# Kernel tuning notes

Measured on AMD Instinct MI355X. Metric: run time of the kernel, lower is better.

## Reference

```python
import jax, jax.numpy as jnp
import numpy as np

BATCH, T, N_INP, N_HID = 32, 512, 128, 1024
DT = 0.042
RHO = 0.99
INPUT_SCALING = 1.0
THRESHOLD = 0.5
RESET = 0.0
R_ = 1.0   # resistance
C_ = 1.0   # capacity
P = 0.5
HARMONIC = N_HID * P          # scalar, as in source: n_hid * p
SPIKING = N_HID - HARMONIC    # scalar, as in source


def setup_inputs() -> dict:
    key = jax.random.key(0)
    k1, k2, k3, k4, k5 = jax.random.split(key, 5)
    x = jax.random.normal(k1, (BATCH, T, N_INP), dtype=jnp.float32)
    # input-to-hidden in (0, input_scaling), per torch.rand * input_scaling
    x2h = jax.random.uniform(k2, (N_INP, N_HID), dtype=jnp.float32) * INPUT_SCALING
    # hidden-to-hidden: full topology, rescaled to spectral radius rho
    W = np.asarray(jax.random.uniform(k3, (N_HID, N_HID), minval=-1.0, maxval=1.0))
    sr = float(np.max(np.abs(np.linalg.eigvals(W))))
    h2h = jnp.asarray(W * (RHO / sr), dtype=jnp.float32)
    # gamma/epsilon sampled per-unit from uniform ranges (tuple branch of __init__)
    gamma = jax.random.uniform(k4, (N_HID,), minval=0.5, maxval=1.5, dtype=jnp.float32)
    epsilon = jax.random.uniform(k5, (N_HID,), minval=0.001, maxval=0.01, dtype=jnp.float32)
    bias = jnp.zeros((N_HID,), dtype=jnp.float32)
    return {"x": x, "x2h": x2h, "h2h": h2h, "gamma": gamma, "epsilon": epsilon, "bias": bias}


def reference(x, x2h, h2h, gamma, epsilon, bias):
    B = x.shape[0]
    dtype = x.dtype
    u_decay = 1.0 - R_ * C_ * DT  # u = u + R*C*dt*(-u)

    def step(carry, xt):
        hy, hz, u = carry
        # spiking_osc: threshold, reset, leak
        spike = (u > THRESHOLD).astype(dtype)
        u = jnp.where(spike == 1.0, RESET, u)
        u = u * u_decay
        # coupled-oscillator update
        drive = jnp.tanh(xt @ x2h + hy @ h2h + bias)
        hz = hz + DT * (drive - gamma * hy - (epsilon * (hz * HARMONIC) + u * SPIKING))
        hy = hy + DT * hz
        return (hy, hz, u), (hy, hz, u, spike)

    zeros = jnp.zeros((B, N_HID), dtype=dtype)
    (_, _, _), (hy_t, hz_t, u_t, spk_t) = jax.lax.scan(
        step, (zeros, zeros, zeros), jnp.swapaxes(x, 0, 1)
    )
    # (T, B, H) -> (B, T, H), matching the per-step lists of the original
    tr = lambda a: jnp.swapaxes(a, 0, 1)
    return tr(hy_t), tr(hz_t), tr(u_t), tr(spk_t)
```

## Files before the change

### kernel.cpp

```cpp
#include <hip/hip_runtime.h>
#include <cmath>

constexpr int  Bn  = 32, Tn = 512, NIn = 128, Hn = 1024;
constexpr long long TH  = (long long)Tn * Hn;
constexpr long long BTH = (long long)Bn * TH;
constexpr float DTc  = 0.042f;
constexpr float UDEC = 1.0f - 1.0f * 1.0f * DTc;
constexpr float HARM = 512.0f;
constexpr float SPIK = 512.0f;

__device__ unsigned g_tag[16 * 32 * 16];

__global__ void init_tag() {
    int i = threadIdx.x;
    __hip_atomic_store(&g_tag[i * 16], 0u,
                       __ATOMIC_RELAXED, __HIP_MEMORY_SCOPE_AGENT);
}

__global__ __launch_bounds__(256) void pre_gemm(const float* __restrict__ x,
                                                const float* __restrict__ x2h,
                                                const float* __restrict__ bias,
                                                float* __restrict__ pre) {
    __shared__ float xs[64 * 128];
    __shared__ float ws[128 * 64];
    const int tid = threadIdx.x;
    const int rb  = blockIdx.y * 64;
    const int cb  = blockIdx.x * 64;

#pragma unroll
    for (int i = 0; i < 8; ++i) {
        int idx = i * 1024 + tid * 4;
        int r = idx >> 7, k = idx & 127;
        *(float4*)(&xs[r * 128 + k]) =
            *(const float4*)(&x[(long long)(rb + r) * NIn + k]);
    }
#pragma unroll
    for (int i = 0; i < 8; ++i) {
        int idx = i * 1024 + tid * 4;
        int k = idx >> 6, c = idx & 63;
        *(float4*)(&ws[k * 64 + c]) =
            *(const float4*)(&x2h[(long long)k * Hn + cb + c]);
    }
    __syncthreads();

    const int tx = tid & 15, ty = tid >> 4;
    const int r0 = ty * 4, c0 = tx * 4;
    float acc[4][4] = {};
#pragma unroll 4
    for (int k = 0; k < 128; ++k) {
        float4 bv = *(const float4*)(&ws[k * 64 + c0]);
        float a0 = xs[(r0 + 0) * 128 + k];
        float a1 = xs[(r0 + 1) * 128 + k];
        float a2 = xs[(r0 + 2) * 128 + k];
        float a3 = xs[(r0 + 3) * 128 + k];
        acc[0][0] += a0 * bv.x; acc[0][1] += a0 * bv.y; acc[0][2] += a0 * bv.z; acc[0][3] += a0 * bv.w;
        acc[1][0] += a1 * bv.x; acc[1][1] += a1 * bv.y; acc[1][2] += a1 * bv.z; acc[1][3] += a1 * bv.w;
        acc[2][0] += a2 * bv.x; acc[2][1] += a2 * bv.y; acc[2][2] += a2 * bv.z; acc[2][3] += a2 * bv.w;
        acc[3][0] += a3 * bv.x; acc[3][1] += a3 * bv.y; acc[3][2] += a3 * bv.z; acc[3][3] += a3 * bv.w;
    }
    float4 bb = *(const float4*)(&bias[cb + c0]);
#pragma unroll
    for (int i = 0; i < 4; ++i) {
        float4 o;
        o.x = acc[i][0] + bb.x; o.y = acc[i][1] + bb.y;
        o.z = acc[i][2] + bb.z; o.w = acc[i][3] + bb.w;
        *(float4*)(&pre[(long long)(rb + r0 + i) * Hn + cb + c0]) = o;
    }
}

__global__ __launch_bounds__(512, 1) void ron_loop8(const float* __restrict__ h2h,
                                                    const float* __restrict__ gam,
                                                    const float* __restrict__ eps,
                                                    float* __restrict__ out) {
    extern __shared__ float sm[];
    float* hyl  = sm;
    float* wt   = sm + 4 * 1028;
    float* part = wt;

    const int tid = threadIdx.x;
    const int bx  = blockIdx.x;
    const int bg  = bx & 7;
    const int hg  = bx >> 3;
    const int c0  = hg * 32;
    const int b0  = bg * 4;
    unsigned* mytag   = &g_tag[(bg * 32 + hg) * 16];
    unsigned* tagbase = &g_tag[bg * 32 * 16];

    float* hy_o = out;
    float* hz_o = out + BTH;
    float* u_o  = out + 2 * BTH;
    float* sp_o = out + 3 * BTH;

    for (int idx = tid; idx < 32 * 1024; idx += 512) {
        int cc2 = idx & 31, k = idx >> 5;
        wt[cc2 * 1028 + k] = h2h[(long long)k * Hn + c0 + cc2];
    }
    __syncthreads();

    const int ks   = tid & 63;
    const int tile = tid >> 6;

    float4 W[4][4];
#pragma unroll
    for (int j = 0; j < 4; ++j)
#pragma unroll
        for (int m = 0; m < 4; ++m)
            W[j][m] = *(const float4*)(wt + (tile * 4 + j) * 1028 + m * 256 + ks * 4);

    const float* hp0 = hyl + ks * 4;
    const float* hp1 = hp0 + 1028;
    const float* hp2 = hp0 + 2 * 1028;
    const float* hp3 = hp0 + 3 * 1028;
    float* pw = part + (tile * 4) * 65 + ks;

    const int r  = tid & 127;
    const int cc = r & 31;
    const int bb = r >> 5;
    const int b  = b0 + bb;
    const int h  = c0 + cc;
    const float g = gam[h];
    const float e = eps[h];
    float hy = 0.0f, hz = 0.0f, u = 0.0f;

#define D4(dst, hv, wv)                                         \
    dst = fmaf(hv.x, wv.x, dst); dst = fmaf(hv.y, wv.y, dst);   \
    dst = fmaf(hv.z, wv.z, dst); dst = fmaf(hv.w, wv.w, dst)

    for (int t = 0; t < Tn; ++t) {
        float pre_v = 0.0f;
        if (tid < 128)
            pre_v = u_o[(long long)b * TH + (long long)t * Hn + h];

        float acc = 0.0f;
        if (t > 0) {
            const long long base = (long long)b0 * TH + (long long)(t - 1) * Hn + tid;
            float v[8];
#pragma unroll
            for (int i = 0; i < 8; ++i) {
                v[i] = __hip_atomic_load(
                    &hy_o[base + (long long)(i >> 1) * TH + (i & 1) * 512],
                    __ATOMIC_RELAXED, __HIP_MEMORY_SCOPE_AGENT);
            }
#pragma unroll
            for (int i = 0; i < 8; ++i)
                hyl[(i >> 1) * 1028 + (i & 1) * 512 + tid] = v[i];
            __syncthreads();

            float a00 = 0.f, a01 = 0.f, a02 = 0.f, a03 = 0.f;
            float a10 = 0.f, a11 = 0.f, a12 = 0.f, a13 = 0.f;
            float a20 = 0.f, a21 = 0.f, a22 = 0.f, a23 = 0.f;
            float a30 = 0.f, a31 = 0.f, a32 = 0.f, a33 = 0.f;
#pragma unroll
            for (int m = 0; m < 4; ++m) {
                const int o4 = m * 256;
                float4 h0 = *(const float4*)(hp0 + o4);
                float4 h1 = *(const float4*)(hp1 + o4);
                float4 h2 = *(const float4*)(hp2 + o4);
                float4 h3 = *(const float4*)(hp3 + o4);
                D4(a00, h0, W[0][m]); D4(a01, h0, W[1][m]); D4(a02, h0, W[2][m]); D4(a03, h0, W[3][m]);
                D4(a10, h1, W[0][m]); D4(a11, h1, W[1][m]); D4(a12, h1, W[2][m]); D4(a13, h1, W[3][m]);
                D4(a20, h2, W[0][m]); D4(a21, h2, W[1][m]); D4(a22, h2, W[2][m]); D4(a23, h2, W[3][m]);
                D4(a30, h3, W[0][m]); D4(a31, h3, W[1][m]); D4(a32, h3, W[2][m]); D4(a33, h3, W[3][m]);
            }

            pw[(0 * 32 + 0) * 65] = a00; pw[(0 * 32 + 1) * 65] = a01;
            pw[(0 * 32 + 2) * 65] = a02; pw[(0 * 32 + 3) * 65] = a03;
            pw[(1 * 32 + 0) * 65] = a10; pw[(1 * 32 + 1) * 65] = a11;
            pw[(1 * 32 + 2) * 65] = a12; pw[(1 * 32 + 3) * 65] = a13;
            pw[(2 * 32 + 0) * 65] = a20; pw[(2 * 32 + 1) * 65] = a21;
            pw[(2 * 32 + 2) * 65] = a22; pw[(2 * 32 + 3) * 65] = a23;
            pw[(3 * 32 + 0) * 65] = a30; pw[(3 * 32 + 1) * 65] = a31;
            pw[(3 * 32 + 2) * 65] = a32; pw[(3 * 32 + 3) * 65] = a33;
            __syncthreads();

            if (tid < 128) {
                const float* pr = part + r * 65;
                float s0 = 0.f, s1 = 0.f, s2 = 0.f, s3 = 0.f;
#pragma unroll
                for (int k = 0; k < 64; k += 4) {
                    s0 += pr[k + 0]; s1 += pr[k + 1];
                    s2 += pr[k + 2]; s3 += pr[k + 3];
                }
                acc = (s0 + s1) + (s2 + s3);
            }
        }

        float spike = 0.0f;
        long long o = 0;
        if (tid < 128) {
            spike = (u > 0.5f) ? 1.0f : 0.0f;
            u = (spike == 1.0f) ? 0.0f : u;
            u = u * UDEC;
            float drive = tanhf(acc + pre_v);
            hz = hz + DTc * (drive - g * hy - (e * (hz * HARM) + u * SPIK));
            hy = hy + DTc * hz;
            o = (long long)b * TH + (long long)t * Hn + h;
            __hip_atomic_store(&hy_o[o], hy,
                               __ATOMIC_RELAXED, __HIP_MEMORY_SCOPE_AGENT);
        }

        if (t < Tn - 1) {
            __syncthreads();
            if (tid == 0)
                __hip_atomic_store(mytag, (unsigned)(t + 1),
                                   __ATOMIC_RELAXED, __HIP_MEMORY_SCOPE_AGENT);
        }

        if (tid < 128) {
            hz_o[o] = hz;
            u_o[o]  = u;
            sp_o[o] = spike;
        }

        if (t < Tn - 1) {
            if (tid < 64) {
                const unsigned target = (unsigned)(t + 1);
                const int idx = tid & 31;
                for (;;) {
                    unsigned v = __hip_atomic_load(&tagbase[idx * 16],
                                                   __ATOMIC_RELAXED,
                                                   __HIP_MEMORY_SCOPE_AGENT);
                    if (__ballot(v < target) == 0ull) break;
                }
            }
            __syncthreads();
        }
    }
#undef D4
}

__global__ __launch_bounds__(256, 1) void ron_loop4(const float* __restrict__ h2h,
                                                    const float* __restrict__ gam,
                                                    const float* __restrict__ eps,
                                                    float* __restrict__ out) {
    extern __shared__ float sm[];
    float* hyl  = sm;
    float* wt   = sm + 4 * 1028;
    float* part = wt;

    const int tid = threadIdx.x;
    const int bx  = blockIdx.x;
    const int bg  = bx & 7;
    const int hg  = bx >> 3;
    const int c0  = hg * 32;
    const int b0  = bg * 4;
    unsigned* mytag   = &g_tag[(bg * 32 + hg) * 16];
    unsigned* tagbase = &g_tag[bg * 32 * 16];

    float* hy_o = out;
    float* hz_o = out + BTH;
    float* u_o  = out + 2 * BTH;
    float* sp_o = out + 3 * BTH;

    for (int idx = tid; idx < 32 * 1024; idx += 256) {
        int cc2 = idx & 31, k = idx >> 5;
        wt[cc2 * 1028 + k] = h2h[(long long)k * Hn + c0 + cc2];
    }
    __syncthreads();

    const int ks   = tid & 31;
    const int tile = tid >> 5;

    float4 W[4][8];
#pragma unroll
    for (int j = 0; j < 4; ++j)
#pragma unroll
        for (int m = 0; m < 8; ++m)
            W[j][m] = *(const float4*)(wt + (tile * 4 + j) * 1028 + (ks + 32 * m) * 4);

    const float* hp0 = hyl + ks * 4;
    const float* hp1 = hp0 + 1028;
    const float* hp2 = hp0 + 2 * 1028;
    const float* hp3 = hp0 + 3 * 1028;
    float* pw = part + (tile * 4) * 33 + ks;

    const int r  = tid & 127;
    const int cc = r & 31;
    const int bb = r >> 5;
    const int b  = b0 + bb;
    const int h  = c0 + cc;
    const float g = gam[h];
    const float e = eps[h];
    float hy = 0.0f, hz = 0.0f, u = 0.0f;

#define D4(dst, hv, wv)                                         \
    dst = fmaf(hv.x, wv.x, dst); dst = fmaf(hv.y, wv.y, dst);   \
    dst = fmaf(hv.z, wv.z, dst); dst = fmaf(hv.w, wv.w, dst)

    for (int t = 0; t < Tn; ++t) {
        float pre_v = 0.0f;
        if (tid < 128)
            pre_v = u_o[(long long)b * TH + (long long)t * Hn + h];

        float acc = 0.0f;
        if (t > 0) {
            const long long base = (long long)b0 * TH + (long long)(t - 1) * Hn + tid;
            float v[16];
#pragma unroll
            for (int i = 0; i < 16; ++i) {
                v[i] = __hip_atomic_load(
                    &hy_o[base + (long long)(i >> 2) * TH + (i & 3) * 256],
                    __ATOMIC_RELAXED, __HIP_MEMORY_SCOPE_AGENT);
            }
#pragma unroll
            for (int i = 0; i < 16; ++i)
                hyl[(i >> 2) * 1028 + (i & 3) * 256 + tid] = v[i];
            __syncthreads();

            float a00 = 0.f, a01 = 0.f, a02 = 0.f, a03 = 0.f;
            float a10 = 0.f, a11 = 0.f, a12 = 0.f, a13 = 0.f;
            float a20 = 0.f, a21 = 0.f, a22 = 0.f, a23 = 0.f;
            float a30 = 0.f, a31 = 0.f, a32 = 0.f, a33 = 0.f;
#pragma unroll
            for (int m = 0; m < 8; ++m) {
                const int o4 = m * 128;
                float4 h0 = *(const float4*)(hp0 + o4);
                float4 h1 = *(const float4*)(hp1 + o4);
                float4 h2 = *(const float4*)(hp2 + o4);
                float4 h3 = *(const float4*)(hp3 + o4);
                D4(a00, h0, W[0][m]); D4(a01, h0, W[1][m]); D4(a02, h0, W[2][m]); D4(a03, h0, W[3][m]);
                D4(a10, h1, W[0][m]); D4(a11, h1, W[1][m]); D4(a12, h1, W[2][m]); D4(a13, h1, W[3][m]);
                D4(a20, h2, W[0][m]); D4(a21, h2, W[1][m]); D4(a22, h2, W[2][m]); D4(a23, h2, W[3][m]);
                D4(a30, h3, W[0][m]); D4(a31, h3, W[1][m]); D4(a32, h3, W[2][m]); D4(a33, h3, W[3][m]);
            }

            pw[(0 * 32 + 0) * 33] = a00; pw[(0 * 32 + 1) * 33] = a01;
            pw[(0 * 32 + 2) * 33] = a02; pw[(0 * 32 + 3) * 33] = a03;
            pw[(1 * 32 + 0) * 33] = a10; pw[(1 * 32 + 1) * 33] = a11;
            pw[(1 * 32 + 2) * 33] = a12; pw[(1 * 32 + 3) * 33] = a13;
            pw[(2 * 32 + 0) * 33] = a20; pw[(2 * 32 + 1) * 33] = a21;
            pw[(2 * 32 + 2) * 33] = a22; pw[(2 * 32 + 3) * 33] = a23;
            pw[(3 * 32 + 0) * 33] = a30; pw[(3 * 32 + 1) * 33] = a31;
            pw[(3 * 32 + 2) * 33] = a32; pw[(3 * 32 + 3) * 33] = a33;
            __syncthreads();

            if (tid < 128) {
                const float* pr = part + r * 33;
                float s0 = 0.f, s1 = 0.f, s2 = 0.f, s3 = 0.f;
#pragma unroll
                for (int k = 0; k < 32; k += 4) {
                    s0 += pr[k + 0]; s1 += pr[k + 1];
                    s2 += pr[k + 2]; s3 += pr[k + 3];
                }
                acc = (s0 + s1) + (s2 + s3);
            }
        }

        float spike = 0.0f;
        long long o = 0;
        if (tid < 128) {
            spike = (u > 0.5f) ? 1.0f : 0.0f;
            u = (spike == 1.0f) ? 0.0f : u;
            u = u * UDEC;
            float drive = tanhf(acc + pre_v);
            hz = hz + DTc * (drive - g * hy - (e * (hz * HARM) + u * SPIK));
            hy = hy + DTc * hz;
            o = (long long)b * TH + (long long)t * Hn + h;
            __hip_atomic_store(&hy_o[o], hy,
                               __ATOMIC_RELAXED, __HIP_MEMORY_SCOPE_AGENT);
        }

        if (t < Tn - 1) {
            __syncthreads();
            if (tid == 0)
                __hip_atomic_store(mytag, (unsigned)(t + 1),
                                   __ATOMIC_RELAXED, __HIP_MEMORY_SCOPE_AGENT);
        }

        if (tid < 128) {
            hz_o[o] = hz;
            u_o[o]  = u;
            sp_o[o] = spike;
        }

        if (t < Tn - 1) {
            if (tid < 64) {
                const unsigned target = (unsigned)(t + 1);
                const int idx = tid & 31;
                for (;;) {
                    unsigned v = __hip_atomic_load(&tagbase[idx * 16],
                                                   __ATOMIC_RELAXED,
                                                   __HIP_MEMORY_SCOPE_AGENT);
                    if (__ballot(v < target) == 0ull) break;
                    __builtin_amdgcn_s_sleep(1);
                }
            }
            __syncthreads();
        }
    }
#undef D4
}

extern "C" void kernel_launch(void* const* d_in, const int* in_sizes, int n_in,
                              void* d_out, int out_size, void* d_ws, size_t ws_size,
                              hipStream_t stream) {
    const float* x    = (const float*)d_in[0];
    const float* x2h  = (const float*)d_in[1];
    const float* h2h  = (const float*)d_in[2];
    const float* gam  = (const float*)d_in[3];
    const float* eps  = (const float*)d_in[4];
    const float* bias = (const float*)d_in[5];
    float* out = (float*)d_out;
    float* pre = out + 2 * BTH;

    init_tag<<<1, 512, 0, stream>>>();
    pre_gemm<<<dim3(16, 256), dim3(256), 0, stream>>>(x, x2h, bias, pre);

    const unsigned smem = (4 * 1028 + 32 * 1028) * sizeof(float);
    (void)hipFuncSetAttribute((const void*)ron_loop8,
                              hipFuncAttributeMaxDynamicSharedMemorySize,
                              (int)smem);
    (void)hipFuncSetAttribute((const void*)ron_loop4,
                              hipFuncAttributeMaxDynamicSharedMemorySize,
                              (int)smem);

    void* args[] = {(void*)&h2h, (void*)&gam, (void*)&eps, (void*)&out};

    bool launched =
        (hipLaunchCooperativeKernel((void*)ron_loop8, dim3(256), dim3(512),
                                    args, smem, stream) == hipSuccess);
    if (!launched) {
        (void)hipLaunchCooperativeKernel((void*)ron_loop4, dim3(256),
                                         dim3(256), args, smem, stream);
    }
}
```

Measured before the change: 1.961 ms.

## Replace tag barrier with per-element tagged hy exchange buffer

```diff
diff --git a/kernel.cpp b/kernel.cpp
--- a/kernel.cpp
+++ b/kernel.cpp
@@ -9,12 +9,16 @@
 constexpr float HARM = 512.0f;
 constexpr float SPIK = 512.0f;
 
+__device__ unsigned long long g_ex[2][8][4][1024];
+
 __device__ unsigned g_tag[16 * 32 * 16];
 
-__global__ void init_tag() {
-    int i = threadIdx.x;
-    __hip_atomic_store(&g_tag[i * 16], 0u,
-                       __ATOMIC_RELAXED, __HIP_MEMORY_SCOPE_AGENT);
+__global__ void init_ex() {
+    int i = blockIdx.x * 256 + threadIdx.x;
+    ((unsigned long long*)g_ex)[i] = 0xFFFFFFFF00000000ULL;
+    if (i < 16 * 32)
+        __hip_atomic_store(&g_tag[i * 16], 0u,
+                           __ATOMIC_RELAXED, __HIP_MEMORY_SCOPE_AGENT);
 }
 
 __global__ __launch_bounds__(256) void pre_gemm(const float* __restrict__ x,
@@ -68,6 +72,167 @@
     }
 }
 
+__global__ __launch_bounds__(512, 1) void ron_fuse(const float* __restrict__ h2h,
+                                                   const float* __restrict__ gam,
+                                                   const float* __restrict__ eps,
+                                                   float* __restrict__ out) {
+    extern __shared__ float sm[];
+    float* hyl  = sm;
+    float* wt   = sm + 4 * 1028;
+    float* part = wt;
+
+    const int tid = threadIdx.x;
+    const int bx  = blockIdx.x;
+    const int bg  = bx & 7;
+    const int hg  = bx >> 3;
+    const int c0  = hg * 32;
+    const int b0  = bg * 4;
+
+    float* hy_o = out;
+    float* hz_o = out + BTH;
+    float* u_o  = out + 2 * BTH;
+    float* sp_o = out + 3 * BTH;
+
+    for (int idx = tid; idx < 32 * 1024; idx += 512) {
+        int cc2 = idx & 31, k = idx >> 5;
+        wt[cc2 * 1028 + k] = h2h[(long long)k * Hn + c0 + cc2];
+    }
+    __syncthreads();
+
+    const int ks   = tid & 63;
+    const int tile = tid >> 6;
+
+    float4 W[4][4];
+#pragma unroll
+    for (int j = 0; j < 4; ++j)
+#pragma unroll
+        for (int m = 0; m < 4; ++m)
+            W[j][m] = *(const float4*)(wt + (tile * 4 + j) * 1028 + m * 256 + ks * 4);
+
+    const float* hp0 = hyl + ks * 4;
+    const float* hp1 = hp0 + 1028;
+    const float* hp2 = hp0 + 2 * 1028;
+    const float* hp3 = hp0 + 3 * 1028;
+    float* pw = part + (tile * 4) * 65 + ks;
+
+    const int r  = tid & 127;
+    const int cc = r & 31;
+    const int bb = r >> 5;
+    const int b  = b0 + bb;
+    const int h  = c0 + cc;
+    const float g = gam[h];
+    const float e = eps[h];
+    float hy = 0.0f, hz = 0.0f, u = 0.0f;
+
+#define D4(dst, hv, wv)                                         \
+    dst = fmaf(hv.x, wv.x, dst); dst = fmaf(hv.y, wv.y, dst);   \
+    dst = fmaf(hv.z, wv.z, dst); dst = fmaf(hv.w, wv.w, dst)
+
+    for (int t = 0; t < Tn; ++t) {
+        float pre_v = 0.0f;
+        if (tid < 128)
+            pre_v = u_o[(long long)b * TH + (long long)t * Hn + h];
+
+        float acc = 0.0f;
+        if (t > 0) {
+            const int par = (t - 1) & 1;
+            const unsigned want = (unsigned)(t - 1);
+            unsigned long long w[8];
+            float fv[8];
+            unsigned got = 0;
+#pragma unroll
+            for (int i = 0; i < 8; ++i)
+                w[i] = __hip_atomic_load(
+                    &g_ex[par][bg][i >> 1][(i & 1) * 512 + tid],
+                    __ATOMIC_RELAXED, __HIP_MEMORY_SCOPE_AGENT);
+#pragma unroll
+            for (int i = 0; i < 8; ++i)
+                if ((unsigned)(w[i] >> 32) == want) {
+                    fv[i] = __uint_as_float((unsigned)w[i]);
+                    got |= 1u << i;
+                }
+            while (got != 0xFFu) {
+#pragma unroll
+                for (int i = 0; i < 8; ++i) {
+                    if (!(got & (1u << i))) {
+                        unsigned long long v = __hip_atomic_load(
+                            &g_ex[par][bg][i >> 1][(i & 1) * 512 + tid],
+                            __ATOMIC_RELAXED, __HIP_MEMORY_SCOPE_AGENT);
+                        if ((unsigned)(v >> 32) == want) {
+                            fv[i] = __uint_as_float((unsigned)v);
+                            got |= 1u << i;
+                        }
+                    }
+                }
+            }
+#pragma unroll
+            for (int i = 0; i < 8; ++i)
+                hyl[(i >> 1) * 1028 + (i & 1) * 512 + tid] = fv[i];
+            __syncthreads();
+
+            float a00 = 0.f, a01 = 0.f, a02 = 0.f, a03 = 0.f;
+            float a10 = 0.f, a11 = 0.f, a12 = 0.f, a13 = 0.f;
+            float a20 = 0.f, a21 = 0.f, a22 = 0.f, a23 = 0.f;
+            float a30 = 0.f, a31 = 0.f, a32 = 0.f, a33 = 0.f;
+#pragma unroll
+            for (int m = 0; m < 4; ++m) {
+                const int o4 = m * 256;
+                float4 h0 = *(const float4*)(hp0 + o4);
+                float4 h1 = *(const float4*)(hp1 + o4);
+                float4 h2 = *(const float4*)(hp2 + o4);
+                float4 h3 = *(const float4*)(hp3 + o4);
+                D4(a00, h0, W[0][m]); D4(a01, h0, W[1][m]); D4(a02, h0, W[2][m]); D4(a03, h0, W[3][m]);
+                D4(a10, h1, W[0][m]); D4(a11, h1, W[1][m]); D4(a12, h1, W[2][m]); D4(a13, h1, W[3][m]);
+                D4(a20, h2, W[0][m]); D4(a21, h2, W[1][m]); D4(a22, h2, W[2][m]); D4(a23, h2, W[3][m]);
+                D4(a30, h3, W[0][m]); D4(a31, h3, W[1][m]); D4(a32, h3, W[2][m]); D4(a33, h3, W[3][m]);
+            }
+
+            pw[(0 * 32 + 0) * 65] = a00; pw[(0 * 32 + 1) * 65] = a01;
+            pw[(0 * 32 + 2) * 65] = a02; pw[(0 * 32 + 3) * 65] = a03;
+            pw[(1 * 32 + 0) * 65] = a10; pw[(1 * 32 + 1) * 65] = a11;
+            pw[(1 * 32 + 2) * 65] = a12; pw[(1 * 32 + 3) * 65] = a13;
+            pw[(2 * 32 + 0) * 65] = a20; pw[(2 * 32 + 1) * 65] = a21;
+            pw[(2 * 32 + 2) * 65] = a22; pw[(2 * 32 + 3) * 65] = a23;
+            pw[(3 * 32 + 0) * 65] = a30; pw[(3 * 32 + 1) * 65] = a31;
+            pw[(3 * 32 + 2) * 65] = a32; pw[(3 * 32 + 3) * 65] = a33;
+            __syncthreads();
+
+            if (tid < 128) {
+                const float* pr = part + r * 65;
+                float s0 = 0.f, s1 = 0.f, s2 = 0.f, s3 = 0.f;
+#pragma unroll
+                for (int k = 0; k < 64; k += 4) {
+                    s0 += pr[k + 0]; s1 += pr[k + 1];
+                    s2 += pr[k + 2]; s3 += pr[k + 3];
+                }
+                acc = (s0 + s1) + (s2 + s3);
+            }
+        }
+
+        if (tid < 128) {
+            float spike = (u > 0.5f) ? 1.0f : 0.0f;
+            u = (spike == 1.0f) ? 0.0f : u;
+            u = u * UDEC;
+            float drive = tanhf(acc + pre_v);
+            hz = hz + DTc * (drive - g * hy - (e * (hz * HARM) + u * SPIK));
+            hy = hy + DTc * hz;
+            if (t < Tn - 1) {
+                unsigned long long pk =
+                    ((unsigned long long)(unsigned)t << 32) |
+                    (unsigned long long)__float_as_uint(hy);
+                __hip_atomic_store(&g_ex[t & 1][bg][bb][h], pk,
+                                   __ATOMIC_RELAXED, __HIP_MEMORY_SCOPE_AGENT);
+            }
+            const long long o = (long long)b * TH + (long long)t * Hn + h;
+            hy_o[o] = hy;
+            hz_o[o] = hz;
+            u_o[o]  = u;
+            sp_o[o] = spike;
+        }
+    }
+#undef D4
+}
+
 __global__ __launch_bounds__(512, 1) void ron_loop8(const float* __restrict__ h2h,
                                                     const float* __restrict__ gam,
                                                     const float* __restrict__ eps,
@@ -229,168 +394,6 @@
 #undef D4
 }
 
-__global__ __launch_bounds__(256, 1) void ron_loop4(const float* __restrict__ h2h,
-                                                    const float* __restrict__ gam,
-                                                    const float* __restrict__ eps,
-                                                    float* __restrict__ out) {
-    extern __shared__ float sm[];
-    float* hyl  = sm;
-    float* wt   = sm + 4 * 1028;
-    float* part = wt;
-
-    const int tid = threadIdx.x;
-    const int bx  = blockIdx.x;
-    const int bg  = bx & 7;
-    const int hg  = bx >> 3;
-    const int c0  = hg * 32;
-    const int b0  = bg * 4;
-    unsigned* mytag   = &g_tag[(bg * 32 + hg) * 16];
-    unsigned* tagbase = &g_tag[bg * 32 * 16];
-
-    float* hy_o = out;
-    float* hz_o = out + BTH;
-    float* u_o  = out + 2 * BTH;
-    float* sp_o = out + 3 * BTH;
-
-    for (int idx = tid; idx < 32 * 1024; idx += 256) {
-        int cc2 = idx & 31, k = idx >> 5;
-        wt[cc2 * 1028 + k] = h2h[(long long)k * Hn + c0 + cc2];
-    }
-    __syncthreads();
-
-    const int ks   = tid & 31;
-    const int tile = tid >> 5;
-
-    float4 W[4][8];
-#pragma unroll
-    for (int j = 0; j < 4; ++j)
-#pragma unroll
-        for (int m = 0; m < 8; ++m)
-            W[j][m] = *(const float4*)(wt + (tile * 4 + j) * 1028 + (ks + 32 * m) * 4);
-
-    const float* hp0 = hyl + ks * 4;
-    const float* hp1 = hp0 + 1028;
-    const float* hp2 = hp0 + 2 * 1028;
-    const float* hp3 = hp0 + 3 * 1028;
-    float* pw = part + (tile * 4) * 33 + ks;
-
-    const int r  = tid & 127;
-    const int cc = r & 31;
-    const int bb = r >> 5;
-    const int b  = b0 + bb;
-    const int h  = c0 + cc;
-    const float g = gam[h];
-    const float e = eps[h];
-    float hy = 0.0f, hz = 0.0f, u = 0.0f;
-
-#define D4(dst, hv, wv)                                         \
-    dst = fmaf(hv.x, wv.x, dst); dst = fmaf(hv.y, wv.y, dst);   \
-    dst = fmaf(hv.z, wv.z, dst); dst = fmaf(hv.w, wv.w, dst)
-
-    for (int t = 0; t < Tn; ++t) {
-        float pre_v = 0.0f;
-        if (tid < 128)
-            pre_v = u_o[(long long)b * TH + (long long)t * Hn + h];
-
-        float acc = 0.0f;
-        if (t > 0) {
-            const long long base = (long long)b0 * TH + (long long)(t - 1) * Hn + tid;
-            float v[16];
-#pragma unroll
-            for (int i = 0; i < 16; ++i) {
-                v[i] = __hip_atomic_load(
-                    &hy_o[base + (long long)(i >> 2) * TH + (i & 3) * 256],
-                    __ATOMIC_RELAXED, __HIP_MEMORY_SCOPE_AGENT);
-            }
-#pragma unroll
-            for (int i = 0; i < 16; ++i)
-                hyl[(i >> 2) * 1028 + (i & 3) * 256 + tid] = v[i];
-            __syncthreads();
-
-            float a00 = 0.f, a01 = 0.f, a02 = 0.f, a03 = 0.f;
-            float a10 = 0.f, a11 = 0.f, a12 = 0.f, a13 = 0.f;
-            float a20 = 0.f, a21 = 0.f, a22 = 0.f, a23 = 0.f;
-            float a30 = 0.f, a31 = 0.f, a32 = 0.f, a33 = 0.f;
-#pragma unroll
-            for (int m = 0; m < 8; ++m) {
-                const int o4 = m * 128;
-                float4 h0 = *(const float4*)(hp0 + o4);
-                float4 h1 = *(const float4*)(hp1 + o4);
-                float4 h2 = *(const float4*)(hp2 + o4);
-                float4 h3 = *(const float4*)(hp3 + o4);
-                D4(a00, h0, W[0][m]); D4(a01, h0, W[1][m]); D4(a02, h0, W[2][m]); D4(a03, h0, W[3][m]);
-                D4(a10, h1, W[0][m]); D4(a11, h1, W[1][m]); D4(a12, h1, W[2][m]); D4(a13, h1, W[3][m]);
-                D4(a20, h2, W[0][m]); D4(a21, h2, W[1][m]); D4(a22, h2, W[2][m]); D4(a23, h2, W[3][m]);
-                D4(a30, h3, W[0][m]); D4(a31, h3, W[1][m]); D4(a32, h3, W[2][m]); D4(a33, h3, W[3][m]);
-            }
-
-            pw[(0 * 32 + 0) * 33] = a00; pw[(0 * 32 + 1) * 33] = a01;
-            pw[(0 * 32 + 2) * 33] = a02; pw[(0 * 32 + 3) * 33] = a03;
-            pw[(1 * 32 + 0) * 33] = a10; pw[(1 * 32 + 1) * 33] = a11;
-            pw[(1 * 32 + 2) * 33] = a12; pw[(1 * 32 + 3) * 33] = a13;
-            pw[(2 * 32 + 0) * 33] = a20; pw[(2 * 32 + 1) * 33] = a21;
-            pw[(2 * 32 + 2) * 33] = a22; pw[(2 * 32 + 3) * 33] = a23;
-            pw[(3 * 32 + 0) * 33] = a30; pw[(3 * 32 + 1) * 33] = a31;
-            pw[(3 * 32 + 2) * 33] = a32; pw[(3 * 32 + 3) * 33] = a33;
-            __syncthreads();
-
-            if (tid < 128) {
-                const float* pr = part + r * 33;
-                float s0 = 0.f, s1 = 0.f, s2 = 0.f, s3 = 0.f;
-#pragma unroll
-                for (int k = 0; k < 32; k += 4) {
-                    s0 += pr[k + 0]; s1 += pr[k + 1];
-                    s2 += pr[k + 2]; s3 += pr[k + 3];
-                }
-                acc = (s0 + s1) + (s2 + s3);
-            }
-        }
-
-        float spike = 0.0f;
-        long long o = 0;
-        if (tid < 128) {
-            spike = (u > 0.5f) ? 1.0f : 0.0f;
-            u = (spike == 1.0f) ? 0.0f : u;
-            u = u * UDEC;
-            float drive = tanhf(acc + pre_v);
-            hz = hz + DTc * (drive - g * hy - (e * (hz * HARM) + u * SPIK));
-            hy = hy + DTc * hz;
-            o = (long long)b * TH + (long long)t * Hn + h;
-            __hip_atomic_store(&hy_o[o], hy,
-                               __ATOMIC_RELAXED, __HIP_MEMORY_SCOPE_AGENT);
-        }
-
-        if (t < Tn - 1) {
-            __syncthreads();
-            if (tid == 0)
-                __hip_atomic_store(mytag, (unsigned)(t + 1),
-                                   __ATOMIC_RELAXED, __HIP_MEMORY_SCOPE_AGENT);
-        }
-
-        if (tid < 128) {
-            hz_o[o] = hz;
-            u_o[o]  = u;
-            sp_o[o] = spike;
-        }
-
-        if (t < Tn - 1) {
-            if (tid < 64) {
-                const unsigned target = (unsigned)(t + 1);
-                const int idx = tid & 31;
-                for (;;) {
-                    unsigned v = __hip_atomic_load(&tagbase[idx * 16],
-                                                   __ATOMIC_RELAXED,
-                                                   __HIP_MEMORY_SCOPE_AGENT);
-                    if (__ballot(v < target) == 0ull) break;
-                    __builtin_amdgcn_s_sleep(1);
-                }
-            }
-            __syncthreads();
-        }
-    }
-#undef D4
-}
-
 extern "C" void kernel_launch(void* const* d_in, const int* in_sizes, int n_in,
                               void* d_out, int out_size, void* d_ws, size_t ws_size,
                               hipStream_t stream) {
@@ -403,24 +406,24 @@
     float* out = (float*)d_out;
     float* pre = out + 2 * BTH;
 
-    init_tag<<<1, 512, 0, stream>>>();
+    init_ex<<<256, 256, 0, stream>>>();
     pre_gemm<<<dim3(16, 256), dim3(256), 0, stream>>>(x, x2h, bias, pre);
 
     const unsigned smem = (4 * 1028 + 32 * 1028) * sizeof(float);
+    (void)hipFuncSetAttribute((const void*)ron_fuse,
+                              hipFuncAttributeMaxDynamicSharedMemorySize,
+                              (int)smem);
     (void)hipFuncSetAttribute((const void*)ron_loop8,
                               hipFuncAttributeMaxDynamicSharedMemorySize,
                               (int)smem);
-    (void)hipFuncSetAttribute((const void*)ron_loop4,
-                              hipFuncAttributeMaxDynamicSharedMemorySize,
-                              (int)smem);
 
     void* args[] = {(void*)&h2h, (void*)&gam, (void*)&eps, (void*)&out};
 
     bool launched =
-        (hipLaunchCooperativeKernel((void*)ron_loop8, dim3(256), dim3(512),
+        (hipLaunchCooperativeKernel((void*)ron_fuse, dim3(256), dim3(512),
                                     args, smem, stream) == hipSuccess);
     if (!launched) {
-        (void)hipLaunchCooperativeKernel((void*)ron_loop4, dim3(256),
-                                         dim3(256), args, smem, stream);
+        (void)hipLaunchCooperativeKernel((void*)ron_loop8, dim3(256),
+                                         dim3(512), args, smem, stream);
     }
 }
```

Result: slower. 2.826 ms (+44.1%).
